# Optimization experiments

Hardware: AMD Instinct MI355X
Metric: run time of the kernel (lower is better)

## Reference

```python
import jax, jax.numpy as jnp
import numpy as np

EPS = 1e-08


def setup_inputs() -> dict:
    key = jax.random.key(0)
    N, D = 8192, 384
    student_output = jax.random.normal(key, (N, D), dtype=jnp.float32)
    return {"student_output": student_output}


def reference(student_output):
    # L2-normalize rows (F.normalize with eps clamp on the norm)
    norm = jnp.linalg.norm(student_output, axis=-1, keepdims=True)
    x = student_output / jnp.maximum(norm, EPS)  # [N, D]

    n = x.shape[0]
    dots = x @ x.T                               # [N, N] cosine similarities
    # mask self-similarity on the diagonal with -1
    diag = jnp.arange(n)
    dots = dots.at[diag, diag].set(-1.0)

    indices = jnp.argmax(dots, axis=1)           # 1-NN per row
    nn_x = jnp.take(x, indices, axis=0)          # [N, D]

    # torch PairwiseDistance(p=2, eps=1e-8): ||x - y + eps||_2
    distances = jnp.linalg.norm(x - nn_x + EPS, axis=-1)  # [N]
    loss = -jnp.mean(jnp.log(distances + EPS))
    return loss
```

## Files before the change

### kernel.cpp

```cpp
#include <hip/hip_runtime.h>
#include <hip/hip_bf16.h>
#include <math.h>

#define D 384
#define EPS 1e-8f

#define RPB 256
#define CPS 512
#define POS_W 128
#define NPOS 4
#define NKB 6
#define NT  24
#define STG 24576

typedef int    intx4   __attribute__((ext_vector_type(4)));

__global__ __launch_bounds__(256) void prep_kernel(const float* __restrict__ in,
                                                   float* __restrict__ rnorm,
                                                   char* __restrict__ xq,
                                                   unsigned long long* __restrict__ best,
                                                   float* __restrict__ out, int N) {
    if (blockIdx.x == 0 && threadIdx.x == 0) *out = 0.f;
    int row = blockIdx.x * 4 + (threadIdx.x >> 6);
    if (row >= N) return;
    int lane = threadIdx.x & 63;
    const float* p = in + (size_t)row * D;
    float4 a = *(const float4*)(p + lane * 4);
    float2 b = *(const float2*)(p + 256 + lane * 2);
    float s = a.x * a.x + a.y * a.y + a.z * a.z + a.w * a.w + b.x * b.x + b.y * b.y;
#pragma unroll
    for (int off = 32; off >= 1; off >>= 1) s += __shfl_xor(s, off, 64);
    float rn = 1.0f / fmaxf(sqrtf(s), EPS);
    if (lane == 0) { rnorm[row] = rn; best[row] = 0ull; }
    const float sc = rn * 127.f;
    int b0 = __float2int_rn(a.x * sc), b1 = __float2int_rn(a.y * sc);
    int b2 = __float2int_rn(a.z * sc), b3 = __float2int_rn(a.w * sc);
    int b4 = __float2int_rn(b.x * sc), b5 = __float2int_rn(b.y * sc);
    char* q = xq + (size_t)row * D;
    *(int*)(q + lane * 4) = (b0 & 0xff) | ((b1 & 0xff) << 8) | ((b2 & 0xff) << 16) | (b3 << 24);
    *(short*)(q + 256 + lane * 2) = (short)((b4 & 0xff) | (b5 << 8));
}

__global__ __launch_bounds__(256, 2) void maxdot_rows(const char* __restrict__ xq,
                                                      unsigned long long* __restrict__ best) {
    __shared__ char Bs[3][STG];

    const int t    = threadIdx.x;
    const int lane = t & 63;
    const int wv   = t >> 6;
    const int quad = lane >> 4, l16 = lane & 15;
    const int rb   = blockIdx.x >> 4;
    const int cs   = blockIdx.x & 15;
    const int row0b = rb * RPB;
    const int col0s = cs * CPS;
    const int wrow0 = row0b + wv * 64;

    intx4 acc[4][8];
#pragma unroll
    for (int mi = 0; mi < 4; ++mi)
#pragma unroll
        for (int ni = 0; ni < 8; ++ni) acc[mi][ni] = (intx4){0, 0, 0, 0};

    int rv[16];
    int ri[16];
#pragma unroll
    for (int i = 0; i < 16; ++i) { rv[i] = -0x7fffffff; ri[i] = 0; }

    const int sc = t >> 2;
    const int sg = t & 3;

#define GLDS(SRC, DST) __builtin_amdgcn_global_load_lds(                               \
        (const __attribute__((address_space(1))) void*)(SRC),                          \
        (__attribute__((address_space(3))) void*)(DST), 16, 0, 0)

#define STAGE(TT, BUF) do {                                                            \
        const int p_  = (TT) / NKB, kb_ = (TT) - p_ * NKB;                             \
        const int cb_ = col0s + p_ * POS_W;                                            \
        const size_t ko_ = (size_t)kb_ * 64 + sg * 16;                                 \
        GLDS(xq + (size_t)(cb_ + sc)        * 384 + ko_, (BUF) +         t * 16);      \
        GLDS(xq + (size_t)(cb_ + 64 + sc)   * 384 + ko_, (BUF) +  4096 + t * 16);      \
        GLDS(xq + (size_t)(row0b + sc)      * 384 + ko_, (BUF) +  8192 + t * 16);      \
        GLDS(xq + (size_t)(row0b + 64 + sc) * 384 + ko_, (BUF) + 12288 + t * 16);      \
        GLDS(xq + (size_t)(row0b + 128 + sc)* 384 + ko_, (BUF) + 16384 + t * 16);      \
        GLDS(xq + (size_t)(row0b + 192 + sc)* 384 + ko_, (BUF) + 20480 + t * 16);      \
    } while (0)

    STAGE(0, Bs[0]);
    STAGE(1, Bs[1]);

    char* b0 = Bs[0];
    char* b1 = Bs[1];
    char* b2 = Bs[2];

    const int lofs = l16 * 64 + quad * 16;

    for (int tt = 0; tt < NT; ++tt) {
        const int pos = tt / NKB, kb = tt - pos * NKB;
        const int colbase = col0s + pos * POS_W;

        if (tt < NT - 1) asm volatile("s_waitcnt vmcnt(6)" ::: "memory");
        else             asm volatile("s_waitcnt vmcnt(0)" ::: "memory");
        __builtin_amdgcn_s_barrier();
        __builtin_amdgcn_sched_barrier(0);

        if (tt + 2 < NT) STAGE(tt + 2, b2);

        const char* Ab = b0 + 8192 + wv * 4096;
        intx4 af[4];
#pragma unroll
        for (int mi = 0; mi < 4; ++mi)
            af[mi] = *(const intx4*)(Ab + mi * 1024 + lofs);
        intx4 bfr[8];
#pragma unroll
        for (int ni = 0; ni < 8; ++ni)
            bfr[ni] = *(const intx4*)(b0 + ni * 1024 + lofs);
#pragma unroll
        for (int mi = 0; mi < 4; ++mi)
#pragma unroll
            for (int ni = 0; ni < 8; ++ni)
                acc[mi][ni] = __builtin_amdgcn_mfma_i32_16x16x64_i8(af[mi], bfr[ni], acc[mi][ni], 0, 0, 0);

        if (kb == NKB - 1) {
            const bool dg = (colbase < row0b + RPB) && (row0b < colbase + POS_W);
#pragma unroll
            for (int mi = 0; mi < 4; ++mi)
#pragma unroll
                for (int reg = 0; reg < 4; ++reg) {
                    const int r = wrow0 + mi * 16 + quad * 4 + reg;
                    int d[8];
#pragma unroll
                    for (int ni = 0; ni < 8; ++ni) d[ni] = acc[mi][ni][reg];
                    if (dg) {
#pragma unroll
                        for (int ni = 0; ni < 8; ++ni)
                            if (colbase + ni * 16 + l16 == r) d[ni] = -0x40000000;
                    }
                    int m = d[0]; int ci = 0;
#pragma unroll
                    for (int ni = 1; ni < 8; ++ni) {
                        bool gt = d[ni] > m;
                        m  = gt ? d[ni] : m;
                        ci = gt ? ni : ci;
                    }
                    const int slot = mi * 4 + reg;
                    bool upd = m > rv[slot];
                    rv[slot] = upd ? m : rv[slot];
                    ri[slot] = upd ? (colbase + ci * 16 + l16) : ri[slot];
#pragma unroll
                    for (int ni = 0; ni < 8; ++ni) acc[mi][ni][reg] = 0;
                }
        }

        char* tmp = b0; b0 = b1; b1 = b2; b2 = tmp;
    }
#undef STAGE
#undef GLDS

#pragma unroll
    for (int slot = 0; slot < 16; ++slot) {
        int v = rv[slot]; int ci = ri[slot];
#pragma unroll
        for (int m = 1; m < 16; m <<= 1) {
            int ov = __shfl_xor(v, m, 64);
            int oi = __shfl_xor(ci, m, 64);
            bool take = (ov > v) || (ov == v && oi < ci);
            v  = take ? ov : v;
            ci = take ? oi : ci;
        }
        if (l16 == 0) {
            const int r = wrow0 + (slot >> 2) * 16 + quad * 4 + (slot & 3);
            unsigned u = ((unsigned)v) ^ 0x80000000u;
            unsigned long long key = ((unsigned long long)u << 32) | (unsigned)(~ci);
            atomicMax(best + r, key);
        }
    }
}

__global__ __launch_bounds__(256) void loss_kernel(const float* __restrict__ in,
                                                   const float* __restrict__ rnorm,
                                                   const unsigned long long* __restrict__ best,
                                                   float* __restrict__ out, int N) {
    __shared__ float part[4];
    const int wave = threadIdx.x >> 6, lane = threadIdx.x & 63;
    const int gw = blockIdx.x * 4 + wave;
    float local = 0.f;
    for (int row = gw; row < N; row += 1024) {
        unsigned long long key = best[row];
        int j = (int)(~(unsigned)(key & 0xffffffffull));
        float rni = rnorm[row], rnj = rnorm[j];
        const float* pi = in + (size_t)row * D;
        const float* pj = in + (size_t)j * D;
        float s = 0.f;
#pragma unroll
        for (int c = 0; c < 6; ++c) {
            float xi = pi[lane + 64 * c] * rni;
            float xj = pj[lane + 64 * c] * rnj;
            float dvv = xi - xj + EPS;
            s += dvv * dvv;
        }
#pragma unroll
        for (int off = 32; off > 0; off >>= 1) s += __shfl_down(s, off, 64);
        if (lane == 0) local += -logf(sqrtf(s) + EPS);
    }
    if (lane == 0) part[wave] = local;
    __syncthreads();
    if (threadIdx.x == 0)
        atomicAdd(out, (part[0] + part[1] + part[2] + part[3]) / (float)N);
}

extern "C" void kernel_launch(void* const* d_in, const int* in_sizes, int n_in,
                              void* d_out, int out_size, void* d_ws, size_t ws_size,
                              hipStream_t stream) {
    const float* in = (const float*)d_in[0];
    float* out = (float*)d_out;
    const int N = in_sizes[0] / D;

    char* ws = (char*)d_ws;
    float* rnorm = (float*)ws;
    unsigned long long* best = (unsigned long long*)(ws + 64 * 1024);
    char* xq = ws + 192 * 1024;

    prep_kernel<<<N / 4, 256, 0, stream>>>(in, rnorm, xq, best, out, N);
    maxdot_rows<<<512, 256, 0, stream>>>(xq, best);
    loss_kernel<<<256, 256, 0, stream>>>(in, rnorm, best, out, N);
}
```

Baseline: 105.8 us.

## Exploit Gram symmetry for triangular tiles and derive loss from quantized dots

The similarity kernel now uses 128-row blocks and skips tiles below the block diagonal, so roughly half of the int8 MFMA work is avoided. Each computed tile also updates a column-wise argmax through atomicMax, which covers the mirrored rows that were skipped. The loss kernel no longer gathers fp32 rows. It rebuilds each distance as sqrt(2-2c) from the stored int8 dot and per-row inverse quantized norms, which adds quantization error to the distance values and drops the +EPS term from the pairwise distance. More atomics and extra register work per tile are the added cost.

```diff
diff --git a/kernel.cpp b/kernel.cpp
--- a/kernel.cpp
+++ b/kernel.cpp
@@ -5,18 +5,18 @@
 #define D 384
 #define EPS 1e-8f
 
-#define RPB 256
+#define RPB 128
 #define CPS 512
 #define POS_W 128
 #define NPOS 4
 #define NKB 6
 #define NT  24
-#define STG 24576
+#define STG 16384
 
 typedef int    intx4   __attribute__((ext_vector_type(4)));
 
 __global__ __launch_bounds__(256) void prep_kernel(const float* __restrict__ in,
-                                                   float* __restrict__ rnorm,
+                                                   float* __restrict__ qninv,
                                                    char* __restrict__ xq,
                                                    unsigned long long* __restrict__ best,
                                                    float* __restrict__ out, int N) {
@@ -31,7 +31,6 @@
 #pragma unroll
     for (int off = 32; off >= 1; off >>= 1) s += __shfl_xor(s, off, 64);
     float rn = 1.0f / fmaxf(sqrtf(s), EPS);
-    if (lane == 0) { rnorm[row] = rn; best[row] = 0ull; }
     const float sc = rn * 127.f;
     int b0 = __float2int_rn(a.x * sc), b1 = __float2int_rn(a.y * sc);
     int b2 = __float2int_rn(a.z * sc), b3 = __float2int_rn(a.w * sc);
@@ -39,32 +38,38 @@
     char* q = xq + (size_t)row * D;
     *(int*)(q + lane * 4) = (b0 & 0xff) | ((b1 & 0xff) << 8) | ((b2 & 0xff) << 16) | (b3 << 24);
     *(short*)(q + 256 + lane * 2) = (short)((b4 & 0xff) | (b5 << 8));
-}
-
-__global__ __launch_bounds__(256, 2) void maxdot_rows(const char* __restrict__ xq,
+    int qs = b0 * b0 + b1 * b1 + b2 * b2 + b3 * b3 + b4 * b4 + b5 * b5;
+#pragma unroll
+    for (int off = 32; off >= 1; off >>= 1) qs += __shfl_xor(qs, off, 64);
+    if (lane == 0) { qninv[row] = 1.0f / sqrtf((float)qs); best[row] = 0ull; }
+}
+
+__global__ __launch_bounds__(256, 3) void maxdot_rows(const char* __restrict__ xq,
                                                       unsigned long long* __restrict__ best) {
+    const int rb = blockIdx.x >> 4;
+    const int cs = blockIdx.x & 15;
+    if (cs < (rb >> 2)) return;
+
     __shared__ char Bs[3][STG];
 
     const int t    = threadIdx.x;
     const int lane = t & 63;
     const int wv   = t >> 6;
     const int quad = lane >> 4, l16 = lane & 15;
-    const int rb   = blockIdx.x >> 4;
-    const int cs   = blockIdx.x & 15;
     const int row0b = rb * RPB;
     const int col0s = cs * CPS;
-    const int wrow0 = row0b + wv * 64;
-
-    intx4 acc[4][8];
-#pragma unroll
-    for (int mi = 0; mi < 4; ++mi)
+    const int wrow0 = row0b + wv * 32;
+
+    intx4 acc[2][8];
+#pragma unroll
+    for (int mi = 0; mi < 2; ++mi)
 #pragma unroll
         for (int ni = 0; ni < 8; ++ni) acc[mi][ni] = (intx4){0, 0, 0, 0};
 
-    int rv[16];
-    int ri[16];
-#pragma unroll
-    for (int i = 0; i < 16; ++i) { rv[i] = -0x7fffffff; ri[i] = 0; }
+    int rv[8];
+    int ri[8];
+#pragma unroll
+    for (int i = 0; i < 8; ++i) { rv[i] = -0x7fffffff; ri[i] = 0; }
 
     const int sc = t >> 2;
     const int sg = t & 3;
@@ -81,8 +86,6 @@
         GLDS(xq + (size_t)(cb_ + 64 + sc)   * 384 + ko_, (BUF) +  4096 + t * 16);      \
         GLDS(xq + (size_t)(row0b + sc)      * 384 + ko_, (BUF) +  8192 + t * 16);      \
         GLDS(xq + (size_t)(row0b + 64 + sc) * 384 + ko_, (BUF) + 12288 + t * 16);      \
-        GLDS(xq + (size_t)(row0b + 128 + sc)* 384 + ko_, (BUF) + 16384 + t * 16);      \
-        GLDS(xq + (size_t)(row0b + 192 + sc)* 384 + ko_, (BUF) + 20480 + t * 16);      \
     } while (0)
 
     STAGE(0, Bs[0]);
@@ -98,32 +101,35 @@
         const int pos = tt / NKB, kb = tt - pos * NKB;
         const int colbase = col0s + pos * POS_W;
 
-        if (tt < NT - 1) asm volatile("s_waitcnt vmcnt(6)" ::: "memory");
+        if (tt < NT - 1) asm volatile("s_waitcnt vmcnt(4)" ::: "memory");
         else             asm volatile("s_waitcnt vmcnt(0)" ::: "memory");
         __builtin_amdgcn_s_barrier();
         __builtin_amdgcn_sched_barrier(0);
 
         if (tt + 2 < NT) STAGE(tt + 2, b2);
 
-        const char* Ab = b0 + 8192 + wv * 4096;
-        intx4 af[4];
-#pragma unroll
-        for (int mi = 0; mi < 4; ++mi)
+        const char* Ab = b0 + 8192 + wv * 2048;
+        intx4 af[2];
+#pragma unroll
+        for (int mi = 0; mi < 2; ++mi)
             af[mi] = *(const intx4*)(Ab + mi * 1024 + lofs);
         intx4 bfr[8];
 #pragma unroll
         for (int ni = 0; ni < 8; ++ni)
             bfr[ni] = *(const intx4*)(b0 + ni * 1024 + lofs);
 #pragma unroll
-        for (int mi = 0; mi < 4; ++mi)
+        for (int mi = 0; mi < 2; ++mi)
 #pragma unroll
             for (int ni = 0; ni < 8; ++ni)
                 acc[mi][ni] = __builtin_amdgcn_mfma_i32_16x16x64_i8(af[mi], bfr[ni], acc[mi][ni], 0, 0, 0);
 
         if (kb == NKB - 1) {
             const bool dg = (colbase < row0b + RPB) && (row0b < colbase + POS_W);
-#pragma unroll
-            for (int mi = 0; mi < 4; ++mi)
+            int cv[8], cr[8];
+#pragma unroll
+            for (int ni = 0; ni < 8; ++ni) { cv[ni] = -0x7fffffff; cr[ni] = 0; }
+#pragma unroll
+            for (int mi = 0; mi < 2; ++mi)
 #pragma unroll
                 for (int reg = 0; reg < 4; ++reg) {
                     const int r = wrow0 + mi * 16 + quad * 4 + reg;
@@ -147,8 +153,32 @@
                     rv[slot] = upd ? m : rv[slot];
                     ri[slot] = upd ? (colbase + ci * 16 + l16) : ri[slot];
 #pragma unroll
+                    for (int ni = 0; ni < 8; ++ni) {
+                        bool g = d[ni] > cv[ni];
+                        cv[ni] = g ? d[ni] : cv[ni];
+                        cr[ni] = g ? r : cr[ni];
+                    }
+#pragma unroll
                     for (int ni = 0; ni < 8; ++ni) acc[mi][ni][reg] = 0;
                 }
+#pragma unroll
+            for (int ni = 0; ni < 8; ++ni) {
+                int v = cv[ni], r2 = cr[ni];
+#pragma unroll
+                for (int m = 16; m <= 32; m <<= 1) {
+                    int ov = __shfl_xor(v, m, 64);
+                    int orr = __shfl_xor(r2, m, 64);
+                    bool take = (ov > v) || (ov == v && orr < r2);
+                    v  = take ? ov : v;
+                    r2 = take ? orr : r2;
+                }
+                if (quad == 0) {
+                    const int col = colbase + ni * 16 + l16;
+                    unsigned u = ((unsigned)v) ^ 0x80000000u;
+                    unsigned long long key = ((unsigned long long)u << 32) | (unsigned)(~r2);
+                    atomicMax(best + col, key);
+                }
+            }
         }
 
         char* tmp = b0; b0 = b1; b1 = b2; b2 = tmp;
@@ -157,7 +187,7 @@
 #undef GLDS
 
 #pragma unroll
-    for (int slot = 0; slot < 16; ++slot) {
+    for (int slot = 0; slot < 8; ++slot) {
         int v = rv[slot]; int ci = ri[slot];
 #pragma unroll
         for (int m = 1; m < 16; m <<= 1) {
@@ -176,32 +206,24 @@
     }
 }
 
-__global__ __launch_bounds__(256) void loss_kernel(const float* __restrict__ in,
-                                                   const float* __restrict__ rnorm,
+__global__ __launch_bounds__(256) void loss_kernel(const float* __restrict__ qninv,
                                                    const unsigned long long* __restrict__ best,
                                                    float* __restrict__ out, int N) {
     __shared__ float part[4];
     const int wave = threadIdx.x >> 6, lane = threadIdx.x & 63;
-    const int gw = blockIdx.x * 4 + wave;
+    const int gtid = blockIdx.x * 256 + threadIdx.x;
+    const int stride = gridDim.x * 256;
     float local = 0.f;
-    for (int row = gw; row < N; row += 1024) {
+    for (int row = gtid; row < N; row += stride) {
         unsigned long long key = best[row];
         int j = (int)(~(unsigned)(key & 0xffffffffull));
-        float rni = rnorm[row], rnj = rnorm[j];
-        const float* pi = in + (size_t)row * D;
-        const float* pj = in + (size_t)j * D;
-        float s = 0.f;
-#pragma unroll
-        for (int c = 0; c < 6; ++c) {
-            float xi = pi[lane + 64 * c] * rni;
-            float xj = pj[lane + 64 * c] * rnj;
-            float dvv = xi - xj + EPS;
-            s += dvv * dvv;
-        }
-#pragma unroll
-        for (int off = 32; off > 0; off >>= 1) s += __shfl_down(s, off, 64);
-        if (lane == 0) local += -logf(sqrtf(s) + EPS);
+        int v = (int)(((unsigned)(key >> 32)) ^ 0x80000000u);
+        float c = (float)v * qninv[row] * qninv[j];
+        float s = fmaxf(2.f - 2.f * c, 0.f);
+        local += -logf(sqrtf(s) + EPS);
     }
+#pragma unroll
+    for (int off = 32; off > 0; off >>= 1) local += __shfl_down(local, off, 64);
     if (lane == 0) part[wave] = local;
     __syncthreads();
     if (threadIdx.x == 0)
@@ -216,11 +238,11 @@
     const int N = in_sizes[0] / D;
 
     char* ws = (char*)d_ws;
-    float* rnorm = (float*)ws;
+    float* qninv = (float*)ws;
     unsigned long long* best = (unsigned long long*)(ws + 64 * 1024);
     char* xq = ws + 192 * 1024;
 
-    prep_kernel<<<N / 4, 256, 0, stream>>>(in, rnorm, xq, best, out, N);
-    maxdot_rows<<<512, 256, 0, stream>>>(xq, best);
-    loss_kernel<<<256, 256, 0, stream>>>(in, rnorm, best, out, N);
-}
+    prep_kernel<<<N / 4, 256, 0, stream>>>(in, qninv, xq, best, out, N);
+    maxdot_rows<<<1024, 256, 0, stream>>>(xq, best);
+    loss_kernel<<<16, 256, 0, stream>>>(qninv, best, out, N);
+}
```

Result: slower. 121.5 us (+14.9%).

## Derive NN distance from quantized dot and stream A fragments from global

Applied to the files above, without the earlier changes.

The loss kernel no longer gathers fp32 rows. It computes each distance as sqrt(2-2c), where c is the winning int8 dot product rescaled by per-row inverse norms of the quantized vectors computed in prep. This removes a large gather and reduction but approximates the distance using quantized values and drops the +eps inside the norm. Separately, the maxdot kernel loads its row-side A fragments straight from global memory into double-buffered registers instead of staging them in LDS. That shrinks each LDS stage from 24 KB to 8 KB and the global-to-LDS traffic, at the cost of per-wave global loads that must hit in cache.

```diff
diff --git a/kernel.cpp b/kernel.cpp
--- a/kernel.cpp
+++ b/kernel.cpp
@@ -11,12 +11,11 @@
 #define NPOS 4
 #define NKB 6
 #define NT  24
-#define STG 24576
 
 typedef int    intx4   __attribute__((ext_vector_type(4)));
 
 __global__ __launch_bounds__(256) void prep_kernel(const float* __restrict__ in,
-                                                   float* __restrict__ rnorm,
+                                                   float* __restrict__ qninv,
                                                    char* __restrict__ xq,
                                                    unsigned long long* __restrict__ best,
                                                    float* __restrict__ out, int N) {
@@ -31,7 +30,6 @@
 #pragma unroll
     for (int off = 32; off >= 1; off >>= 1) s += __shfl_xor(s, off, 64);
     float rn = 1.0f / fmaxf(sqrtf(s), EPS);
-    if (lane == 0) { rnorm[row] = rn; best[row] = 0ull; }
     const float sc = rn * 127.f;
     int b0 = __float2int_rn(a.x * sc), b1 = __float2int_rn(a.y * sc);
     int b2 = __float2int_rn(a.z * sc), b3 = __float2int_rn(a.w * sc);
@@ -39,11 +37,15 @@
     char* q = xq + (size_t)row * D;
     *(int*)(q + lane * 4) = (b0 & 0xff) | ((b1 & 0xff) << 8) | ((b2 & 0xff) << 16) | (b3 << 24);
     *(short*)(q + 256 + lane * 2) = (short)((b4 & 0xff) | (b5 << 8));
+    int qs = b0 * b0 + b1 * b1 + b2 * b2 + b3 * b3 + b4 * b4 + b5 * b5;
+#pragma unroll
+    for (int off = 32; off >= 1; off >>= 1) qs += __shfl_xor(qs, off, 64);
+    if (lane == 0) { qninv[row] = 1.0f / sqrtf((float)qs); best[row] = 0ull; }
 }
 
 __global__ __launch_bounds__(256, 2) void maxdot_rows(const char* __restrict__ xq,
                                                       unsigned long long* __restrict__ best) {
-    __shared__ char Bs[3][STG];
+    __shared__ char Bs[3][8192];
 
     const int t    = threadIdx.x;
     const int lane = t & 63;
@@ -77,14 +79,22 @@
         const int p_  = (TT) / NKB, kb_ = (TT) - p_ * NKB;                             \
         const int cb_ = col0s + p_ * POS_W;                                            \
         const size_t ko_ = (size_t)kb_ * 64 + sg * 16;                                 \
-        GLDS(xq + (size_t)(cb_ + sc)        * 384 + ko_, (BUF) +         t * 16);      \
-        GLDS(xq + (size_t)(cb_ + 64 + sc)   * 384 + ko_, (BUF) +  4096 + t * 16);      \
-        GLDS(xq + (size_t)(row0b + sc)      * 384 + ko_, (BUF) +  8192 + t * 16);      \
-        GLDS(xq + (size_t)(row0b + 64 + sc) * 384 + ko_, (BUF) + 12288 + t * 16);      \
-        GLDS(xq + (size_t)(row0b + 128 + sc)* 384 + ko_, (BUF) + 16384 + t * 16);      \
-        GLDS(xq + (size_t)(row0b + 192 + sc)* 384 + ko_, (BUF) + 20480 + t * 16);      \
+        GLDS(xq + (size_t)(cb_ + sc)      * 384 + ko_, (BUF) +        t * 16);         \
+        GLDS(xq + (size_t)(cb_ + 64 + sc) * 384 + ko_, (BUF) + 4096 + t * 16);         \
     } while (0)
 
+    const char* aBase = xq + (size_t)(wrow0 + l16) * 384 + quad * 16;
+#define LOADA(KB, AF) do {                                                             \
+        const char* pa_ = aBase + (size_t)(KB) * 64;                                   \
+        AF[0] = *(const intx4*)(pa_);                                                  \
+        AF[1] = *(const intx4*)(pa_ +  6144);                                          \
+        AF[2] = *(const intx4*)(pa_ + 12288);                                          \
+        AF[3] = *(const intx4*)(pa_ + 18432);                                          \
+    } while (0)
+
+    intx4 af0[4], af1[4];
+
+    LOADA(0, af0);
     STAGE(0, Bs[0]);
     STAGE(1, Bs[1]);
 
@@ -94,22 +104,18 @@
 
     const int lofs = l16 * 64 + quad * 16;
 
-    for (int tt = 0; tt < NT; ++tt) {
+    auto body = [&](intx4 (&afc)[4], intx4 (&afn)[4], int tt) {
         const int pos = tt / NKB, kb = tt - pos * NKB;
         const int colbase = col0s + pos * POS_W;
 
-        if (tt < NT - 1) asm volatile("s_waitcnt vmcnt(6)" ::: "memory");
+        if (tt < NT - 1) asm volatile("s_waitcnt vmcnt(2)" ::: "memory");
         else             asm volatile("s_waitcnt vmcnt(0)" ::: "memory");
         __builtin_amdgcn_s_barrier();
         __builtin_amdgcn_sched_barrier(0);
 
+        if (tt + 1 < NT) { const int nkb = (kb + 1 == NKB) ? 0 : kb + 1; LOADA(nkb, afn); }
         if (tt + 2 < NT) STAGE(tt + 2, b2);
 
-        const char* Ab = b0 + 8192 + wv * 4096;
-        intx4 af[4];
-#pragma unroll
-        for (int mi = 0; mi < 4; ++mi)
-            af[mi] = *(const intx4*)(Ab + mi * 1024 + lofs);
         intx4 bfr[8];
 #pragma unroll
         for (int ni = 0; ni < 8; ++ni)
@@ -118,7 +124,7 @@
         for (int mi = 0; mi < 4; ++mi)
 #pragma unroll
             for (int ni = 0; ni < 8; ++ni)
-                acc[mi][ni] = __builtin_amdgcn_mfma_i32_16x16x64_i8(af[mi], bfr[ni], acc[mi][ni], 0, 0, 0);
+                acc[mi][ni] = __builtin_amdgcn_mfma_i32_16x16x64_i8(afc[mi], bfr[ni], acc[mi][ni], 0, 0, 0);
 
         if (kb == NKB - 1) {
             const bool dg = (colbase < row0b + RPB) && (row0b < colbase + POS_W);
@@ -152,8 +158,14 @@
         }
 
         char* tmp = b0; b0 = b1; b1 = b2; b2 = tmp;
+    };
+
+    for (int tt = 0; tt < NT; tt += 2) {
+        body(af0, af1, tt);
+        body(af1, af0, tt + 1);
     }
 #undef STAGE
+#undef LOADA
 #undef GLDS
 
 #pragma unroll
@@ -176,32 +188,24 @@
     }
 }
 
-__global__ __launch_bounds__(256) void loss_kernel(const float* __restrict__ in,
-                                                   const float* __restrict__ rnorm,
+__global__ __launch_bounds__(256) void loss_kernel(const float* __restrict__ qninv,
                                                    const unsigned long long* __restrict__ best,
                                                    float* __restrict__ out, int N) {
     __shared__ float part[4];
     const int wave = threadIdx.x >> 6, lane = threadIdx.x & 63;
-    const int gw = blockIdx.x * 4 + wave;
+    const int gtid = blockIdx.x * 256 + threadIdx.x;
+    const int stride = gridDim.x * 256;
     float local = 0.f;
-    for (int row = gw; row < N; row += 1024) {
+    for (int row = gtid; row < N; row += stride) {
         unsigned long long key = best[row];
         int j = (int)(~(unsigned)(key & 0xffffffffull));
-        float rni = rnorm[row], rnj = rnorm[j];
-        const float* pi = in + (size_t)row * D;
-        const float* pj = in + (size_t)j * D;
-        float s = 0.f;
-#pragma unroll
-        for (int c = 0; c < 6; ++c) {
-            float xi = pi[lane + 64 * c] * rni;
-            float xj = pj[lane + 64 * c] * rnj;
-            float dvv = xi - xj + EPS;
-            s += dvv * dvv;
-        }
-#pragma unroll
-        for (int off = 32; off > 0; off >>= 1) s += __shfl_down(s, off, 64);
-        if (lane == 0) local += -logf(sqrtf(s) + EPS);
+        int v = (int)(((unsigned)(key >> 32)) ^ 0x80000000u);
+        float c = (float)v * qninv[row] * qninv[j];
+        float s = fmaxf(2.f - 2.f * c, 0.f);
+        local += -logf(sqrtf(s) + EPS);
     }
+#pragma unroll
+    for (int off = 32; off > 0; off >>= 1) local += __shfl_down(local, off, 64);
     if (lane == 0) part[wave] = local;
     __syncthreads();
     if (threadIdx.x == 0)
@@ -216,11 +220,11 @@
     const int N = in_sizes[0] / D;
 
     char* ws = (char*)d_ws;
-    float* rnorm = (float*)ws;
+    float* qninv = (float*)ws;
     unsigned long long* best = (unsigned long long*)(ws + 64 * 1024);
     char* xq = ws + 192 * 1024;
 
-    prep_kernel<<<N / 4, 256, 0, stream>>>(in, rnorm, xq, best, out, N);
+    prep_kernel<<<N / 4, 256, 0, stream>>>(in, qninv, xq, best, out, N);
     maxdot_rows<<<512, 256, 0, stream>>>(xq, best);
-    loss_kernel<<<256, 256, 0, stream>>>(in, rnorm, best, out, N);
-}
+    loss_kernel<<<16, 256, 0, stream>>>(qninv, best, out, N);
+}
```

Result: faster. 103.0 us (-2.6%).
